# Kernel tuning notes

Measured on AMD Instinct MI355X. Metric: run time of the kernel, lower is better.

## Reference

```python
import jax, jax.numpy as jnp
import numpy as np

NUM_ITERATIONS = 3


def squash(t, axis=-1):
    # scale * t / sqrt(||t||^2 + eps), scale = ||t||^2 / (1 + ||t||^2)
    sq = jnp.sum(t * t, axis=axis, keepdims=True)
    return (sq / (1.0 + sq)) * t / jnp.sqrt(sq + 1e-8)


def setup_inputs() -> dict:
    key = jax.random.key(0)
    k1, k2 = jax.random.split(key)
    B, C, R, I, O = 128, 10, 8192, 8, 16
    x = jax.random.normal(k1, (B, R, I), dtype=jnp.float32)
    route_weights = jax.random.normal(k2, (C, R, I, O), dtype=jnp.float32) * 0.1
    return {"x": x, "route_weights": route_weights}


def reference(x, route_weights):
    # x: [B, R, I]; route_weights: [C, R, I, O]
    u_hat = jnp.einsum('bri,crio->bcro', x, route_weights)  # [B, C, R, O]
    B, C, R, O = u_hat.shape
    b_ij = jnp.zeros((B, C, R), dtype=u_hat.dtype)
    v_j = None
    for it in range(NUM_ITERATIONS):
        c_ij = jax.nn.softmax(b_ij, axis=1)                 # [B, C, R]
        s_j = jnp.einsum('bcr,bcro->bco', c_ij, u_hat)      # [B, C, O]
        v_j = squash(s_j, axis=-1)                          # [B, C, O]
        if it < NUM_ITERATIONS - 1:
            a_ij = jnp.einsum('bcro,bco->bcr', u_hat, v_j)  # [B, C, R]
            b_ij = b_ij + a_ij
    return v_j
```

## Files before the change

### kernel.cpp

```cpp
#include <hip/hip_runtime.h>
#include <hip/hip_fp16.h>
#include <math.h>

#define B_ 128
#define C_ 10
#define R_ 8192
#define I_ 8
#define O_ 16

typedef __attribute__((ext_vector_type(8))) _Float16 half8;
typedef __attribute__((ext_vector_type(16))) float f32x16;

#define XROW 512
#define WROW 64
#define WZERO 80
#define SBO (C_ * B_ * O_)

__device__ __forceinline__ unsigned pk2(float a, float b) {
    __half2 h = __floats2half2_rn(a, b);
    return *(unsigned*)&h;
}

__global__ __launch_bounds__(256, 4) void fused_iter(const float* __restrict__ x,
                                                     const float* __restrict__ w,
                                                     const float* __restrict__ vsum,
                                                     __half* __restrict__ part,
                                                     int mode) {
    __shared__ unsigned xls[8 * XROW];
    __shared__ unsigned wls[(80 + 1) * WROW];

    const int tid = threadIdx.x;
    const int wave = tid >> 6;
    const int lane = tid & 63;
    const int n = lane & 31;
    const int g = lane >> 5;
    const int rp_m = (lane & 31) >> 4;
    const int o_m = lane & 15;
    const int b = wave * 32 + n;
    const int r0 = blockIdx.x * 8;

#pragma unroll
    for (int k = 0; k < 8; ++k) {
        const int f = k * 256 + tid;
        const int bb = f >> 4;
        const int rr = (f >> 1) & 7;
        const int q = f & 1;
        const float4 v = *(const float4*)(x + ((size_t)bb * R_ + r0 + rr) * 8 + q * 4);
        *(uint2*)(xls + rr * XROW + bb * 4 + q * 2) = make_uint2(pk2(v.x, v.y), pk2(v.z, v.w));
    }
#pragma unroll
    for (int k = 0; k < 5; ++k) {
        const int id = k * 256 + tid;
        const int o = id & 15;
        const int r = (id >> 4) & 7;
        const int c = id >> 7;
        const float* wp = w + ((size_t)(c * R_ + r0 + r) * 8) * 16 + o;
        const float f0 = wp[0],  f1 = wp[16],  f2 = wp[32],  f3 = wp[48];
        const float f4 = wp[64], f5 = wp[80],  f6 = wp[96],  f7 = wp[112];
        *(uint4*)(wls + (c * 8 + r) * WROW + o * 4) =
            make_uint4(pk2(f0, f1), pk2(f2, f3), pk2(f4, f5), pk2(f6, f7));
    }
    if (tid < WROW) wls[WZERO * WROW + tid] = 0u;
    __syncthreads();

    float dacc[8];
#pragma unroll
    for (int j = 0; j < 8; ++j) dacc[j] = 0.f;

    const int act = (g == rp_m);

    if (mode) {
#pragma unroll 1
        for (int c = 0; c < C_; ++c) {
            const float4* vp = (const float4*)(vsum + ((size_t)c * B_ + b) * O_ + 4 * g);
            const float4 va = vp[0];
            const float4 vb = vp[2];
#pragma unroll
            for (int rp = 0; rp < 4; ++rp) {
                const int woff = act ? ((c * 8 + 2 * rp + g) * WROW + o_m * 4)
                                     : (WZERO * WROW);
                const half8 a  = *(const half8*)(wls + woff);
                const half8 xb = *(const half8*)(xls + (2 * rp + g) * XROW + b * 4);
                f32x16 u;
#pragma unroll
                for (int j = 0; j < 16; ++j) u[j] = 0.f;
                u = __builtin_amdgcn_mfma_f32_32x32x16_f16(a, xb, u, 0, 0, 0);
                float p0 = u[0] * va.x + u[1] * va.y + u[2] * va.z + u[3] * va.w
                         + u[4] * vb.x + u[5] * vb.y + u[6] * vb.z + u[7] * vb.w;
                float p1 = u[8] * va.x + u[9] * va.y + u[10] * va.z + u[11] * va.w
                         + u[12] * vb.x + u[13] * vb.y + u[14] * vb.z + u[15] * vb.w;
                p0 += __shfl_xor(p0, 32);
                p1 += __shfl_xor(p1, 32);
                dacc[2 * rp]     += __expf(p0);
                dacc[2 * rp + 1] += __expf(p1);
            }
        }
#pragma unroll
        for (int j = 0; j < 8; ++j) dacc[j] = 1.0f / dacc[j];
    }

#pragma unroll 1
    for (int c = 0; c < C_; ++c) {
        float4 va, vb;
        if (mode) {
            const float4* vp = (const float4*)(vsum + ((size_t)c * B_ + b) * O_ + 4 * g);
            va = vp[0]; vb = vp[2];
        }
        f32x16 acc;
#pragma unroll
        for (int j = 0; j < 16; ++j) acc[j] = 0.f;

#pragma unroll
        for (int rp = 0; rp < 4; ++rp) {
            const int woff = act ? ((c * 8 + 2 * rp + g) * WROW + o_m * 4)
                                 : (WZERO * WROW);
            const half8 a  = *(const half8*)(wls + woff);
            const half8 xb = *(const half8*)(xls + (2 * rp + g) * XROW + b * 4);
            f32x16 u;
#pragma unroll
            for (int j = 0; j < 16; ++j) u[j] = 0.f;
            u = __builtin_amdgcn_mfma_f32_32x32x16_f16(a, xb, u, 0, 0, 0);
            float c0, c1;
            if (mode) {
                float p0 = u[0] * va.x + u[1] * va.y + u[2] * va.z + u[3] * va.w
                         + u[4] * vb.x + u[5] * vb.y + u[6] * vb.z + u[7] * vb.w;
                float p1 = u[8] * va.x + u[9] * va.y + u[10] * va.z + u[11] * va.w
                         + u[12] * vb.x + u[13] * vb.y + u[14] * vb.z + u[15] * vb.w;
                p0 += __shfl_xor(p0, 32);
                p1 += __shfl_xor(p1, 32);
                c0 = __expf(p0) * dacc[2 * rp];
                c1 = __expf(p1) * dacc[2 * rp + 1];
            } else {
                c0 = 0.1f; c1 = 0.1f;
            }
#pragma unroll
            for (int j = 0; j < 8; ++j)  acc[j] += c0 * u[j];
#pragma unroll
            for (int j = 8; j < 16; ++j) acc[j] += c1 * u[j];
        }

        const float f0 = acc[0] + acc[8],  f1 = acc[1] + acc[9];
        const float f2 = acc[2] + acc[10], f3 = acc[3] + acc[11];
        const float f4 = acc[4] + acc[12], f5 = acc[5] + acc[13];
        const float f6 = acc[6] + acc[14], f7 = acc[7] + acc[15];
        __half* pp = part + (((size_t)blockIdx.x * C_ + c) * B_ + b) * O_;
        *(uint2*)(pp + 4 * g)     = make_uint2(pk2(f0, f1), pk2(f2, f3));
        *(uint2*)(pp + 8 + 4 * g) = make_uint2(pk2(f4, f5), pk2(f6, f7));
    }
}

__global__ __launch_bounds__(256) void reduce1(const __half* __restrict__ part,
                                               float* __restrict__ part2) {
    const int t = blockIdx.x * 256 + threadIdx.x;
    const int s0 = blockIdx.y * 64;
    const __half* p = part + (size_t)s0 * SBO + t;
    float sum = 0.f;
#pragma unroll 8
    for (int s = 0; s < 64; ++s)
        sum += __half2float(p[(size_t)s * SBO]);
    part2[(size_t)blockIdx.y * SBO + t] = sum;
}

__global__ __launch_bounds__(256) void finish_pass(const float* __restrict__ part2,
                                                   float* __restrict__ vsum,
                                                   float* __restrict__ out,
                                                   int mode) {
    const int t = blockIdx.x * 256 + threadIdx.x;
    float sum = 0.f;
#pragma unroll
    for (int s = 0; s < 16; ++s)
        sum += part2[(size_t)s * SBO + t];

    float sq = sum * sum;
    sq += __shfl_xor(sq, 1);
    sq += __shfl_xor(sq, 2);
    sq += __shfl_xor(sq, 4);
    sq += __shfl_xor(sq, 8);
    const float scale = sq / ((1.0f + sq) * sqrtf(sq + 1e-8f));
    const float v = scale * sum;

    if (mode == 0) {
        vsum[t] = v;
    } else if (mode == 1) {
        vsum[t] += v;
    } else {
        const int o = t & 15, b = (t >> 4) & 127, c = t >> 11;
        out[((size_t)b * C_ + c) * O_ + o] = v;
    }
}

extern "C" void kernel_launch(void* const* d_in, const int* in_sizes, int n_in,
                              void* d_out, int out_size, void* d_ws, size_t ws_size,
                              hipStream_t stream) {
    const float* x = (const float*)d_in[0];
    const float* w = (const float*)d_in[1];
    float* out = (float*)d_out;

    __half* part = (__half*)d_ws;
    float* part2 = (float*)(part + (size_t)1024 * SBO);
    float* vsum  = part2 + (size_t)16 * SBO;

    const dim3 fgrid(R_ / 8);
    const dim3 rgrid(80, 16);
    const dim3 ggrid(80);

    fused_iter<<<fgrid, 256, 0, stream>>>(x, w, vsum, part, 0);
    reduce1<<<rgrid, 256, 0, stream>>>(part, part2);
    finish_pass<<<ggrid, 256, 0, stream>>>(part2, vsum, out, 0);

    fused_iter<<<fgrid, 256, 0, stream>>>(x, w, vsum, part, 1);
    reduce1<<<rgrid, 256, 0, stream>>>(part, part2);
    finish_pass<<<ggrid, 256, 0, stream>>>(part2, vsum, out, 1);

    fused_iter<<<fgrid, 256, 0, stream>>>(x, w, vsum, part, 1);
    reduce1<<<rgrid, 256, 0, stream>>>(part, part2);
    finish_pass<<<ggrid, 256, 0, stream>>>(part2, vsum, out, 2);
}
```

Measured before the change: 228.3 us.

## Pre-transpose x to fp16 r-major layout and load MFMA operands directly into registers

Adds a transpose kernel that converts x once per call into fp16, laid out as [R][B] with 8-element vectors, so each fused_iter block reads its x fragments with coalesced 16-byte loads straight into registers. This drops the x shared-memory staging and its LDS reads, and removes the repeated fp32 reads and conversion of x across the three iterations. Mode 0 now gets its own path that chains the MFMAs into a single accumulator and scales by 0.1 once. The cost is an extra kernel launch plus a write and re-read of a 16 MB fp16 copy of x in workspace.

```diff
diff --git a/kernel.cpp b/kernel.cpp
--- a/kernel.cpp
+++ b/kernel.cpp
@@ -11,7 +11,6 @@
 typedef __attribute__((ext_vector_type(8))) _Float16 half8;
 typedef __attribute__((ext_vector_type(16))) float f32x16;
 
-#define XROW 512
 #define WROW 64
 #define WZERO 80
 #define SBO (C_ * B_ * O_)
@@ -21,12 +20,33 @@
     return *(unsigned*)&h;
 }
 
-__global__ __launch_bounds__(256, 4) void fused_iter(const float* __restrict__ x,
+__global__ __launch_bounds__(256) void transpose_x(const float* __restrict__ x,
+                                                   uint4* __restrict__ xth) {
+    __shared__ uint4 tile[32][33];
+    const int r0 = blockIdx.x * 32, b0 = blockIdx.y * 32;
+#pragma unroll
+    for (int k = 0; k < 4; ++k) {
+        const int f = k * 256 + threadIdx.x;
+        const int bl = f >> 5, rl = f & 31;
+        const float4* src = (const float4*)(x + ((size_t)(b0 + bl) * R_ + r0 + rl) * 8);
+        const float4 v0 = src[0], v1 = src[1];
+        tile[bl][rl] = make_uint4(pk2(v0.x, v0.y), pk2(v0.z, v0.w),
+                                  pk2(v1.x, v1.y), pk2(v1.z, v1.w));
+    }
+    __syncthreads();
+#pragma unroll
+    for (int k = 0; k < 4; ++k) {
+        const int f = k * 256 + threadIdx.x;
+        const int rl = f >> 5, bl = f & 31;
+        xth[(size_t)(r0 + rl) * B_ + b0 + bl] = tile[bl][rl];
+    }
+}
+
+__global__ __launch_bounds__(256, 4) void fused_iter(const uint4* __restrict__ xth,
                                                      const float* __restrict__ w,
                                                      const float* __restrict__ vsum,
                                                      __half* __restrict__ part,
                                                      int mode) {
-    __shared__ unsigned xls[8 * XROW];
     __shared__ unsigned wls[(80 + 1) * WROW];
 
     const int tid = threadIdx.x;
@@ -39,15 +59,6 @@
     const int b = wave * 32 + n;
     const int r0 = blockIdx.x * 8;
 
-#pragma unroll
-    for (int k = 0; k < 8; ++k) {
-        const int f = k * 256 + tid;
-        const int bb = f >> 4;
-        const int rr = (f >> 1) & 7;
-        const int q = f & 1;
-        const float4 v = *(const float4*)(x + ((size_t)bb * R_ + r0 + rr) * 8 + q * 4);
-        *(uint2*)(xls + rr * XROW + bb * 4 + q * 2) = make_uint2(pk2(v.x, v.y), pk2(v.z, v.w));
-    }
 #pragma unroll
     for (int k = 0; k < 5; ++k) {
         const int id = k * 256 + tid;
@@ -61,13 +72,24 @@
             make_uint4(pk2(f0, f1), pk2(f2, f3), pk2(f4, f5), pk2(f6, f7));
     }
     if (tid < WROW) wls[WZERO * WROW + tid] = 0u;
+
+    half8 xf[4];
+#pragma unroll
+    for (int rp = 0; rp < 4; ++rp) {
+        const uint4 t = xth[(size_t)(r0 + 2 * rp + g) * B_ + b];
+        xf[rp] = *(const half8*)&t;
+    }
     __syncthreads();
 
+    f32x16 Z;
+#pragma unroll
+    for (int j = 0; j < 16; ++j) Z[j] = 0.f;
+
+    const int act = (g == rp_m);
+
     float dacc[8];
 #pragma unroll
     for (int j = 0; j < 8; ++j) dacc[j] = 0.f;
-
-    const int act = (g == rp_m);
 
     if (mode) {
 #pragma unroll 1
@@ -79,12 +101,8 @@
             for (int rp = 0; rp < 4; ++rp) {
                 const int woff = act ? ((c * 8 + 2 * rp + g) * WROW + o_m * 4)
                                      : (WZERO * WROW);
-                const half8 a  = *(const half8*)(wls + woff);
-                const half8 xb = *(const half8*)(xls + (2 * rp + g) * XROW + b * 4);
-                f32x16 u;
-#pragma unroll
-                for (int j = 0; j < 16; ++j) u[j] = 0.f;
-                u = __builtin_amdgcn_mfma_f32_32x32x16_f16(a, xb, u, 0, 0, 0);
+                const half8 a = *(const half8*)(wls + woff);
+                const f32x16 u = __builtin_amdgcn_mfma_f32_32x32x16_f16(a, xf[rp], Z, 0, 0, 0);
                 float p0 = u[0] * va.x + u[1] * va.y + u[2] * va.z + u[3] * va.w
                          + u[4] * vb.x + u[5] * vb.y + u[6] * vb.z + u[7] * vb.w;
                 float p1 = u[8] * va.x + u[9] * va.y + u[10] * va.z + u[11] * va.w
@@ -99,53 +117,60 @@
         for (int j = 0; j < 8; ++j) dacc[j] = 1.0f / dacc[j];
     }
 
+    if (mode) {
 #pragma unroll 1
-    for (int c = 0; c < C_; ++c) {
-        float4 va, vb;
-        if (mode) {
+        for (int c = 0; c < C_; ++c) {
             const float4* vp = (const float4*)(vsum + ((size_t)c * B_ + b) * O_ + 4 * g);
-            va = vp[0]; vb = vp[2];
-        }
-        f32x16 acc;
-#pragma unroll
-        for (int j = 0; j < 16; ++j) acc[j] = 0.f;
-
-#pragma unroll
-        for (int rp = 0; rp < 4; ++rp) {
-            const int woff = act ? ((c * 8 + 2 * rp + g) * WROW + o_m * 4)
-                                 : (WZERO * WROW);
-            const half8 a  = *(const half8*)(wls + woff);
-            const half8 xb = *(const half8*)(xls + (2 * rp + g) * XROW + b * 4);
-            f32x16 u;
-#pragma unroll
-            for (int j = 0; j < 16; ++j) u[j] = 0.f;
-            u = __builtin_amdgcn_mfma_f32_32x32x16_f16(a, xb, u, 0, 0, 0);
-            float c0, c1;
-            if (mode) {
+            const float4 va = vp[0], vb = vp[2];
+            f32x16 acc;
+#pragma unroll
+            for (int j = 0; j < 16; ++j) acc[j] = 0.f;
+#pragma unroll
+            for (int rp = 0; rp < 4; ++rp) {
+                const int woff = act ? ((c * 8 + 2 * rp + g) * WROW + o_m * 4)
+                                     : (WZERO * WROW);
+                const half8 a = *(const half8*)(wls + woff);
+                const f32x16 u = __builtin_amdgcn_mfma_f32_32x32x16_f16(a, xf[rp], Z, 0, 0, 0);
                 float p0 = u[0] * va.x + u[1] * va.y + u[2] * va.z + u[3] * va.w
                          + u[4] * vb.x + u[5] * vb.y + u[6] * vb.z + u[7] * vb.w;
                 float p1 = u[8] * va.x + u[9] * va.y + u[10] * va.z + u[11] * va.w
                          + u[12] * vb.x + u[13] * vb.y + u[14] * vb.z + u[15] * vb.w;
                 p0 += __shfl_xor(p0, 32);
                 p1 += __shfl_xor(p1, 32);
-                c0 = __expf(p0) * dacc[2 * rp];
-                c1 = __expf(p1) * dacc[2 * rp + 1];
-            } else {
-                c0 = 0.1f; c1 = 0.1f;
+                const float c0 = __expf(p0) * dacc[2 * rp];
+                const float c1 = __expf(p1) * dacc[2 * rp + 1];
+#pragma unroll
+                for (int j = 0; j < 8; ++j)  acc[j] += c0 * u[j];
+#pragma unroll
+                for (int j = 8; j < 16; ++j) acc[j] += c1 * u[j];
             }
-#pragma unroll
-            for (int j = 0; j < 8; ++j)  acc[j] += c0 * u[j];
-#pragma unroll
-            for (int j = 8; j < 16; ++j) acc[j] += c1 * u[j];
+            const float f0 = acc[0] + acc[8],  f1 = acc[1] + acc[9];
+            const float f2 = acc[2] + acc[10], f3 = acc[3] + acc[11];
+            const float f4 = acc[4] + acc[12], f5 = acc[5] + acc[13];
+            const float f6 = acc[6] + acc[14], f7 = acc[7] + acc[15];
+            __half* pp = part + (((size_t)blockIdx.x * C_ + c) * B_ + b) * O_;
+            *(uint2*)(pp + 4 * g)     = make_uint2(pk2(f0, f1), pk2(f2, f3));
+            *(uint2*)(pp + 8 + 4 * g) = make_uint2(pk2(f4, f5), pk2(f6, f7));
         }
-
-        const float f0 = acc[0] + acc[8],  f1 = acc[1] + acc[9];
-        const float f2 = acc[2] + acc[10], f3 = acc[3] + acc[11];
-        const float f4 = acc[4] + acc[12], f5 = acc[5] + acc[13];
-        const float f6 = acc[6] + acc[14], f7 = acc[7] + acc[15];
-        __half* pp = part + (((size_t)blockIdx.x * C_ + c) * B_ + b) * O_;
-        *(uint2*)(pp + 4 * g)     = make_uint2(pk2(f0, f1), pk2(f2, f3));
-        *(uint2*)(pp + 8 + 4 * g) = make_uint2(pk2(f4, f5), pk2(f6, f7));
+    } else {
+#pragma unroll 1
+        for (int c = 0; c < C_; ++c) {
+            f32x16 u = Z;
+#pragma unroll
+            for (int rp = 0; rp < 4; ++rp) {
+                const int woff = act ? ((c * 8 + 2 * rp + g) * WROW + o_m * 4)
+                                     : (WZERO * WROW);
+                const half8 a = *(const half8*)(wls + woff);
+                u = __builtin_amdgcn_mfma_f32_32x32x16_f16(a, xf[rp], u, 0, 0, 0);
+            }
+            const float f0 = 0.1f * (u[0] + u[8]),  f1 = 0.1f * (u[1] + u[9]);
+            const float f2 = 0.1f * (u[2] + u[10]), f3 = 0.1f * (u[3] + u[11]);
+            const float f4 = 0.1f * (u[4] + u[12]), f5 = 0.1f * (u[5] + u[13]);
+            const float f6 = 0.1f * (u[6] + u[14]), f7 = 0.1f * (u[7] + u[15]);
+            __half* pp = part + (((size_t)blockIdx.x * C_ + c) * B_ + b) * O_;
+            *(uint2*)(pp + 4 * g)     = make_uint2(pk2(f0, f1), pk2(f2, f3));
+            *(uint2*)(pp + 8 + 4 * g) = make_uint2(pk2(f4, f5), pk2(f6, f7));
+        }
     }
 }
 
@@ -196,23 +221,27 @@
     const float* w = (const float*)d_in[1];
     float* out = (float*)d_out;
 
-    __half* part = (__half*)d_ws;
+    uint4* xth   = (uint4*)d_ws;
+    __half* part = (__half*)(xth + (size_t)R_ * B_);
     float* part2 = (float*)(part + (size_t)1024 * SBO);
     float* vsum  = part2 + (size_t)16 * SBO;
 
+    const dim3 tgrid(R_ / 32, B_ / 32);
     const dim3 fgrid(R_ / 8);
     const dim3 rgrid(80, 16);
     const dim3 ggrid(80);
 
-    fused_iter<<<fgrid, 256, 0, stream>>>(x, w, vsum, part, 0);
+    transpose_x<<<tgrid, 256, 0, stream>>>(x, xth);
+
+    fused_iter<<<fgrid, 256, 0, stream>>>(xth, w, vsum, part, 0);
     reduce1<<<rgrid, 256, 0, stream>>>(part, part2);
     finish_pass<<<ggrid, 256, 0, stream>>>(part2, vsum, out, 0);
 
-    fused_iter<<<fgrid, 256, 0, stream>>>(x, w, vsum, part, 1);
+    fused_iter<<<fgrid, 256, 0, stream>>>(xth, w, vsum, part, 1);
     reduce1<<<rgrid, 256, 0, stream>>>(part, part2);
     finish_pass<<<ggrid, 256, 0, stream>>>(part2, vsum, out, 1);
 
-    fused_iter<<<fgrid, 256, 0, stream>>>(x, w, vsum, part, 1);
+    fused_iter<<<fgrid, 256, 0, stream>>>(xth, w, vsum, part, 1);
     reduce1<<<rgrid, 256, 0, stream>>>(part, part2);
     finish_pass<<<ggrid, 256, 0, stream>>>(part2, vsum, out, 2);
 }
```

Result: slower. 266.2 us (+16.6%).
